# Optimization experiments

Hardware: AMD Instinct MI355X
Metric: run time of the kernel (lower is better)

## Reference

```python
import jax, jax.numpy as jnp
import numpy as np

B, E, CIN, C, PRE, DME, DEN = 8, 64, 128, 128, 128, 32, 32
N_EDGE_TYPES, N_PATH_TYPES = 10, 20


def leaky(v):
    return jnp.where(v >= 0, v, 0.1 * v)


def setup_inputs() -> dict:
    key = jax.random.key(0)
    ks = jax.random.split(key, 30)
    s = 0.05
    inp = {
        'x': jax.random.normal(ks[0], (B, CIN, E), jnp.float32),
        'y': jax.random.normal(ks[1], (B, CIN, E), jnp.float32),
        'm_bias_mat': jax.random.normal(ks[2], (B, E, E), jnp.float32),
        'edge_mat': jax.random.randint(ks[3], (B, E, E), 0, N_EDGE_TYPES),
        'p_bias_mat': jax.random.normal(ks[4], (B, E, E, E), jnp.float32),
        'path_mat': jax.random.randint(ks[5], (B, E, E, E), 0, N_PATH_TYPES),
        'pre_out': jax.random.normal(ks[6], (B, PRE, E, E), jnp.float32),
        # parameters (conv1d/conv2d k=1 weights squeezed to matrices/vectors)
        'xc1_w': jax.random.normal(ks[7], (C, CIN), jnp.float32) * s,
        'yc1_w': jax.random.normal(ks[8], (C, CIN), jnp.float32) * s,
        'xc2_w': jax.random.normal(ks[9], (C,), jnp.float32) * s,
        'xc2_b': jax.random.normal(ks[10], (1,), jnp.float32) * s,
        'yc2_w': jax.random.normal(ks[11], (C,), jnp.float32) * s,
        'yc2_b': jax.random.normal(ks[12], (1,), jnp.float32) * s,
        'pconv_w': jax.random.normal(ks[13], (DEN,), jnp.float32) * s,
        'econv_w': jax.random.normal(ks[14], (DME,), jnp.float32) * s,
        'conv1_w': jax.random.normal(ks[15], (C, 2 * C + PRE), jnp.float32) * s,
        'conv1_b': jax.random.normal(ks[16], (C,), jnp.float32) * s,
        'conv2_w': jax.random.normal(ks[17], (C, C, 3, 3), jnp.float32) * s,
        'conv2_b': jax.random.normal(ks[18], (C,), jnp.float32) * s,
        'score_w': jax.random.normal(ks[19], (C,), jnp.float32) * s,
        'xlin_w': jax.random.normal(ks[20], (CIN, CIN), jnp.float32) * s,
        'ylin_w': jax.random.normal(ks[21], (CIN, CIN), jnp.float32) * s,
        'edge_table': jax.random.normal(ks[22], (N_EDGE_TYPES, DME), jnp.float32) * s,
        'path_table': jax.random.normal(ks[23], (N_PATH_TYPES, DEN), jnp.float32) * s,
    }
    return inp


def reference(x, y, m_bias_mat, edge_mat, p_bias_mat, path_mat, pre_out,
              xc1_w, yc1_w, xc2_w, xc2_b, yc2_w, yc2_b, pconv_w, econv_w,
              conv1_w, conv1_b, conv2_w, conv2_b, score_w, xlin_w, ylin_w,
              edge_table, path_table):
    # x,y: [B, CIN, E]; M == N == entity_num == E (required by path_fea reshape)
    x_f = jnp.einsum('ci,bim->bcm', xc1_w, x)                    # [B,C,M]
    y_f = jnp.einsum('ci,bin->bcn', yc1_w, y)                    # [B,C,N]
    x_self = jnp.einsum('c,bcm->bm', xc2_w, x_f) + xc2_b         # [B,M]
    y_other = jnp.einsum('c,bcn->bn', yc2_w, y_f) + yc2_b        # [B,N]
    # torch broadcast: [B,1,M] + [B,N,1] -> [B,N,M]
    logist = leaky(x_self[:, None, :] + y_other[:, :, None])     # [B,E,E]

    # ---- per-entity path attention (vectorized over entity axis e) ----
    path_embed = path_table[path_mat]                            # [B,E,M,N,DEN]
    path_logist = leaky(jnp.einsum('bemnd,d->bemn', path_embed, pconv_w))
    local = logist[:, None, :, :] + path_logist + p_bias_mat     # [B,E,M,N]
    A = jax.nn.softmax(local, axis=-1)
    x_ret = leaky(jnp.einsum('bemn,bcn->bcem', A, y_f) + x_f[:, :, None, :])  # [B,C,E,M]
    A2 = jax.nn.softmax(jnp.swapaxes(local, 2, 3), axis=-1)
    y_ret = leaky(jnp.einsum('benm,bcm->bcen', A2, x_f) + y_f[:, :, None, :])  # [B,C,E,N]
    path_fea = jnp.concatenate([x_ret, y_ret], axis=1)           # [B,2C,E,E]

    men = jnp.concatenate([path_fea, pre_out], axis=1)           # [B,2C+PRE,E,E]
    h = leaky(jnp.einsum('oc,bcij->boij', conv1_w, men) + conv1_b[None, :, None, None])
    h = jax.lax.conv_general_dilated(h, conv2_w, (1, 1), 'SAME',
                                     dimension_numbers=('NCHW', 'OIHW', 'NCHW'))
    men2rel = leaky(h + conv2_b[None, :, None, None])            # [B,C,E,E]

    scores = leaky(jnp.einsum('c,bcij->bij', score_w, men2rel))  # [B,E,E]
    edge_logist = leaky(jnp.einsum('bmnd,d->bmn', edge_table[edge_mat], econv_w))
    g = logist + scores + edge_logist + m_bias_mat               # [B,E,E]

    x_lin = jnp.einsum('ij,bjm->bmi', xlin_w, x)                 # [B,M,CIN]
    y_lin = jnp.einsum('ij,bjn->bni', ylin_w, y)                 # [B,N,CIN]
    G = jax.nn.softmax(g, axis=-1)
    out_x = jnp.einsum('bmn,bni->bim', G, y_lin) + x             # residual, [B,CIN,M]
    G2 = jax.nn.softmax(jnp.swapaxes(g, 1, 2), axis=-1)
    out_y = jnp.einsum('bnm,bmi->bin', G2, x_lin) + y            # [B,CIN,N]
    return (out_x, out_y, men2rel)
```

## Files before the change

kernel.cpp:

```cpp
#include <hip/hip_runtime.h>
#include <hip/hip_bf16.h>


typedef unsigned short u16;
typedef unsigned int u32;
typedef short s16x8 __attribute__((ext_vector_type(8)));
typedef float f32x4 __attribute__((ext_vector_type(4)));

#define NB 8
#define NE 64
#define NC 128

__device__ __forceinline__ float b2f(u16 u) { return __uint_as_float(((u32)u) << 16); }
__device__ __forceinline__ u16 f2b(float f) {
    u32 x = __float_as_uint(f);
    u32 r = (x + 0x7fffu + ((x >> 16) & 1u)) >> 16;
    return (u16)r;
}
__device__ __forceinline__ float lk(float v) { return v >= 0.f ? v : 0.1f * v; }

__global__ __launch_bounds__(256) void k_prepw(const float* __restrict__ w1, const float* __restrict__ w2,
                                               u16* __restrict__ wA1, u16* __restrict__ wA2) {
    int idx = blockIdx.x * 256 + threadIdx.x;
    if (idx < 49152) {
        int e = idx & 7, lane = (idx >> 3) & 63, mtg = (idx >> 9) & 7, kc = idx >> 12;
        int o = mtg * 16 + (lane & 15), c = kc * 32 + ((lane >> 4) << 3) + e;
        wA1[idx] = f2b(w1[o * 384 + c]);
    } else {
        int id2 = idx - 49152;
        if (id2 < 147456) {
            int e = id2 & 7, lane = (id2 >> 3) & 63, mtg = (id2 >> 9) & 7;
            int kc = (id2 >> 12) & 3, tap = id2 >> 14;
            int o = mtg * 16 + (lane & 15), c = kc * 32 + ((lane >> 4) << 3) + e;
            wA2[id2] = f2b(w2[(o * 128 + c) * 9 + tap]);
        }
    }
}

__global__ __launch_bounds__(64) void k_feat(const float* __restrict__ x, const float* __restrict__ y,
                                             const float* __restrict__ xc1, const float* __restrict__ yc1,
                                             u16* __restrict__ xfb, u16* __restrict__ yfb) {
    int blk = blockIdx.x;
    int which = blk >> 10; int r = blk & 1023;
    int b = r >> 7, c = r & 127;
    const float* in = which ? y : x;
    const float* w = which ? yc1 : xc1;
    u16* out = which ? yfb : xfb;
    int m = threadIdx.x;
    const float* wr = w + c * NC;
    const float* ib = in + b * NC * NE + m;
    float acc = 0.f;
#pragma unroll 8
    for (int i = 0; i < NC; ++i) acc += wr[i] * ib[i * NE];
    out[(b * NC + c) * NE + m] = f2b(acc);
}

__global__ __launch_bounds__(256) void k_transf(const u16* __restrict__ xfb, const u16* __restrict__ yfb,
                                                float* __restrict__ xfT, float* __restrict__ yfT) {
    int blk = blockIdx.x;
    int which = blk >> 3, b = blk & 7;
    const u16* src = which ? yfb : xfb;
    float* dst = which ? yfT : xfT;
    int t = threadIdx.x;
    int m = t >> 2, cq = t & 3;
    for (int o = 0; o < 8; ++o) {
        int c0 = cq * 32 + o * 4;
        float4 v;
        v.x = b2f(src[(b * 128 + c0 + 0) * 64 + m]);
        v.y = b2f(src[(b * 128 + c0 + 1) * 64 + m]);
        v.z = b2f(src[(b * 128 + c0 + 2) * 64 + m]);
        v.w = b2f(src[(b * 128 + c0 + 3) * 64 + m]);
        *(float4*)(dst + (b * 64 + m) * 128 + c0) = v;
    }
}

__global__ __launch_bounds__(128) void k_lin(const float* __restrict__ x, const float* __restrict__ y,
                                             const float* __restrict__ xlw, const float* __restrict__ ylw,
                                             float* __restrict__ xl, float* __restrict__ yl) {
    int blk = blockIdx.x;
    int which = blk >> 9; int r = blk & 511;
    int b = r >> 6, ent = r & 63;
    const float* in = which ? y : x;
    const float* w = which ? ylw : xlw;
    float* out = which ? yl : xl;
    int i = threadIdx.x;
    float acc = 0.f;
#pragma unroll 4
    for (int j = 0; j < NC; ++j) acc += w[i * NC + j] * in[(b * NC + j) * NE + ent];
    out[(b * NE + ent) * NC + i] = acc;
}

__global__ __launch_bounds__(64) void k_selfother(const float* __restrict__ xfT, const float* __restrict__ yfT,
                                                  const float* __restrict__ xc2w, const float* __restrict__ xc2b,
                                                  const float* __restrict__ yc2w, const float* __restrict__ yc2b,
                                                  const float* __restrict__ etab, const float* __restrict__ econv,
                                                  const int* __restrict__ edge_mat, const float* __restrict__ m_bias,
                                                  float* __restrict__ Lw, float* __restrict__ gb) {
    int b = blockIdx.x >> 3, ig = blockIdx.x & 7;
    int t = threadIdx.x;
    __shared__ float sXs[64], sYo[64], sEd[16];
    const float* xr = xfT + (b * 64 + t) * 128;
    const float* yr = yfT + (b * 64 + t) * 128;
    float ax = 0.f, ay = 0.f;
#pragma unroll 4
    for (int c = 0; c < NC; ++c) {
        ax += xc2w[c] * xr[c];
        ay += yc2w[c] * yr[c];
    }
    sXs[t] = ax + xc2b[0];
    sYo[t] = ay + yc2b[0];
    if (t < 10) {
        float s = 0.f;
        for (int d = 0; d < 32; ++d) s += etab[t * 32 + d] * econv[d];
        sEd[t] = lk(s);
    }
    __syncthreads();
    for (int ii = 0; ii < 8; ++ii) {
        int i = ig * 8 + ii;
        int idx = (b * NE + i) * NE + t;
        float L = lk(sXs[t] + sYo[i]);
        Lw[idx] = L;
        gb[idx] = L + sEd[edge_mat[idx]] + m_bias[idx];
    }
}

__global__ __launch_bounds__(256) void k_attn(const float* __restrict__ Lw,
                                              const u16* __restrict__ xfb, const u16* __restrict__ yfb,
                                              const float* __restrict__ xfT, const float* __restrict__ yfT,
                                              const int* __restrict__ path_mat, const float* __restrict__ p_bias,
                                              const float* __restrict__ ptab, const float* __restrict__ pconv,
                                              u16* __restrict__ menT) {
    int b = blockIdx.x >> 6, e = blockIdx.x & 63;
    int t = threadIdx.x;
    int lane = t & 63, w = t >> 6;
    __shared__ float sA[64][68];
    __shared__ u16 Abf[64][72];
    __shared__ u16 E2bf[64][72];
    __shared__ float sRed[256];
    __shared__ float sPdot[20];

    if (t < 20) {
        float s = 0.f;
        for (int d = 0; d < 32; ++d) s += ptab[t * 32 + d] * pconv[d];
        sPdot[t] = lk(s);
    }
    __syncthreads();

    {
        int m = t >> 2, n0 = (t & 3) * 16;
        int base = (((b * 64 + e) * 64 + m) * 64 + n0);
        const int4* pm4 = (const int4*)(path_mat + base);
        const float4* pb4 = (const float4*)(p_bias + base);
        const float4* L4 = (const float4*)(Lw + (b * 64 + m) * 64 + n0);
#pragma unroll
        for (int q = 0; q < 4; ++q) {
            int4 pm = pm4[q]; float4 pb = pb4[q]; float4 l = L4[q];
            float4 v;
            v.x = l.x + sPdot[pm.x] + pb.x;
            v.y = l.y + sPdot[pm.y] + pb.y;
            v.z = l.z + sPdot[pm.z] + pb.z;
            v.w = l.w + sPdot[pm.w] + pb.w;
            *(float4*)&sA[m][n0 + q * 4] = v;
        }
    }
    __syncthreads();

    if (t < 128) {
        int r = t >> 1, h = t & 1;
        const float4* rp = (const float4*)&sA[r][h * 32];
        float mx = -1e30f;
#pragma unroll
        for (int k = 0; k < 8; ++k) {
            float4 v = rp[k];
            mx = fmaxf(mx, fmaxf(fmaxf(v.x, v.y), fmaxf(v.z, v.w)));
        }
        mx = fmaxf(mx, __shfl_xor(mx, 1));
        float s = 0.f;
#pragma unroll
        for (int k = 0; k < 8; ++k) {
            float4 v = rp[k];
            s += __expf(v.x - mx) + __expf(v.y - mx) + __expf(v.z - mx) + __expf(v.w - mx);
        }
        s += __shfl_xor(s, 1);
        if (h == 0) { sRed[r] = mx; sRed[64 + r] = 1.f / s; }
    } else {
        int n = (t - 128) >> 1, h = t & 1;
        float mx = -1e30f;
#pragma unroll
        for (int k = 0; k < 32; ++k) mx = fmaxf(mx, sA[h * 32 + k][n]);
        mx = fmaxf(mx, __shfl_xor(mx, 1));
        float s = 0.f;
#pragma unroll
        for (int k = 0; k < 32; ++k) s += __expf(sA[h * 32 + k][n] - mx);
        s += __shfl_xor(s, 1);
        if (h == 0) { sRed[128 + n] = mx; sRed[192 + n] = 1.f / s; }
    }
    __syncthreads();

    {
        int m = t >> 2, q = t & 3;
        float rmax = sRed[m], rinv = sRed[64 + m];
        const float4* rp = (const float4*)&sA[m][q * 16];
        s16x8 pk[2];
#pragma unroll
        for (int g = 0; g < 2; ++g) {
            float4 v0 = rp[g * 2], v1 = rp[g * 2 + 1];
            pk[g][0] = (short)f2b(__expf(v0.x - rmax) * rinv);
            pk[g][1] = (short)f2b(__expf(v0.y - rmax) * rinv);
            pk[g][2] = (short)f2b(__expf(v0.z - rmax) * rinv);
            pk[g][3] = (short)f2b(__expf(v0.w - rmax) * rinv);
            pk[g][4] = (short)f2b(__expf(v1.x - rmax) * rinv);
            pk[g][5] = (short)f2b(__expf(v1.y - rmax) * rinv);
            pk[g][6] = (short)f2b(__expf(v1.z - rmax) * rinv);
            pk[g][7] = (short)f2b(__expf(v1.w - rmax) * rinv);
            *(s16x8*)&Abf[m][q * 16 + g * 8] = pk[g];
        }
    }
    {
        int n = t >> 2, q = t & 3;
        float cmax = sRed[128 + n], cinv = sRed[192 + n];
        s16x8 pk[2];
#pragma unroll
        for (int g = 0; g < 2; ++g) {
#pragma unroll
            for (int k = 0; k < 8; ++k) {
                float v = sA[q * 16 + g * 8 + k][n];
                pk[g][k] = (short)f2b(__expf(v - cmax) * cinv);
            }
            *(s16x8*)&E2bf[n][q * 16 + g * 8] = pk[g];
        }
    }
    __syncthreads();

    int l15 = lane & 15, q4 = (lane >> 4);
    {
        f32x4 acc[2][4];
#pragma unroll
        for (int ci = 0; ci < 2; ++ci)
#pragma unroll
            for (int mt = 0; mt < 4; ++mt) acc[ci][mt] = (f32x4)(0.f);
#pragma unroll
        for (int kt = 0; kt < 2; ++kt) {
            s16x8 afr[2];
#pragma unroll
            for (int ci = 0; ci < 2; ++ci) {
                int c = (2 * w + ci) * 16 + l15;
                afr[ci] = *(const s16x8*)(yfb + (b * 128 + c) * 64 + kt * 32 + q4 * 8);
            }
            s16x8 bfr[4];
#pragma unroll
            for (int mt = 0; mt < 4; ++mt)
                bfr[mt] = *(const s16x8*)&Abf[mt * 16 + l15][kt * 32 + q4 * 8];
#pragma unroll
            for (int ci = 0; ci < 2; ++ci)
#pragma unroll
                for (int mt = 0; mt < 4; ++mt)
                    acc[ci][mt] = __builtin_amdgcn_mfma_f32_16x16x32_bf16(afr[ci], bfr[mt], acc[ci][mt], 0, 0, 0);
        }
#pragma unroll
        for (int ci = 0; ci < 2; ++ci) {
            int c0 = (2 * w + ci) * 16 + q4 * 4;
#pragma unroll
            for (int mt = 0; mt < 4; ++mt) {
                int m = mt * 16 + l15;
                float4 res = *(const float4*)(xfT + (b * 64 + m) * 128 + c0);
                f32x4 a = acc[ci][mt];
                u32 lo = (u32)f2b(lk(a[0] + res.x)) | ((u32)f2b(lk(a[1] + res.y)) << 16);
                u32 hi = (u32)f2b(lk(a[2] + res.z)) | ((u32)f2b(lk(a[3] + res.w)) << 16);
                *(uint2*)(menT + ((b * 64 + e) * 64 + m) * 384 + c0) = make_uint2(lo, hi);
            }
        }
    }
    {
        f32x4 acc[2][4];
#pragma unroll
        for (int ci = 0; ci < 2; ++ci)
#pragma unroll
            for (int nt = 0; nt < 4; ++nt) acc[ci][nt] = (f32x4)(0.f);
#pragma unroll
        for (int kt = 0; kt < 2; ++kt) {
            s16x8 afr[2];
#pragma unroll
            for (int ci = 0; ci < 2; ++ci) {
                int c = (2 * w + ci) * 16 + l15;
                afr[ci] = *(const s16x8*)(xfb + (b * 128 + c) * 64 + kt * 32 + q4 * 8);
            }
            s16x8 bfr[4];
#pragma unroll
            for (int nt = 0; nt < 4; ++nt)
                bfr[nt] = *(const s16x8*)&E2bf[nt * 16 + l15][kt * 32 + q4 * 8];
#pragma unroll
            for (int ci = 0; ci < 2; ++ci)
#pragma unroll
                for (int nt = 0; nt < 4; ++nt)
                    acc[ci][nt] = __builtin_amdgcn_mfma_f32_16x16x32_bf16(afr[ci], bfr[nt], acc[ci][nt], 0, 0, 0);
        }
#pragma unroll
        for (int ci = 0; ci < 2; ++ci) {
            int c0 = (2 * w + ci) * 16 + q4 * 4;
#pragma unroll
            for (int nt = 0; nt < 4; ++nt) {
                int n = nt * 16 + l15;
                float4 res = *(const float4*)(yfT + (b * 64 + n) * 128 + c0);
                f32x4 a = acc[ci][nt];
                u32 lo = (u32)f2b(lk(a[0] + res.x)) | ((u32)f2b(lk(a[1] + res.y)) << 16);
                u32 hi = (u32)f2b(lk(a[2] + res.z)) | ((u32)f2b(lk(a[3] + res.w)) << 16);
                *(uint2*)(menT + ((b * 64 + e) * 64 + n) * 384 + 128 + c0) = make_uint2(lo, hi);
            }
        }
    }
}

__global__ __launch_bounds__(256) void k_prepre(const float* __restrict__ pre, u16* __restrict__ menT) {
    int b = blockIdx.x >> 6, i = blockIdx.x & 63;
    int t = threadIdx.x;
    int j = t & 63, pg = t >> 6;
#pragma unroll
    for (int oc = 0; oc < 4; ++oc) {
        int p0 = pg * 32 + oc * 8;
        s16x8 v;
#pragma unroll
        for (int k = 0; k < 8; ++k)
            v[k] = (short)f2b(pre[((b * 128 + p0 + k) * 64 + i) * 64 + j]);
        *(s16x8*)(menT + ((b * 64 + i) * 64 + j) * 384 + 256 + p0) = v;
    }
}

__global__ __launch_bounds__(256) void k_conv1(const u16* __restrict__ menT, const u16* __restrict__ wA1,
                                               const float* __restrict__ b1, u16* __restrict__ hT) {
    int b = blockIdx.x >> 6, i = blockIdx.x & 63;
    int t = threadIdx.x;
    int lane = t & 63, w = t >> 6, wm = w & 1, wn = w >> 1;
    int l15 = lane & 15, q4 = lane >> 4;

    f32x4 acc[4][2];
#pragma unroll
    for (int mt = 0; mt < 4; ++mt)
#pragma unroll
        for (int nt = 0; nt < 2; ++nt) acc[mt][nt] = (f32x4)(0.f);

    const u16* mrow = menT + (b * 64 + i) * 64 * 384;
    for (int kc = 0; kc < 12; ++kc) {
        s16x8 af[4];
#pragma unroll
        for (int mt = 0; mt < 4; ++mt)
            af[mt] = *(const s16x8*)(wA1 + (((kc * 8 + wm * 4 + mt) * 64 + lane) << 3));
        s16x8 bf[2];
#pragma unroll
        for (int nt = 0; nt < 2; ++nt) {
            int j = (wn * 2 + nt) * 16 + l15;
            bf[nt] = *(const s16x8*)(mrow + j * 384 + kc * 32 + q4 * 8);
        }
#pragma unroll
        for (int mt = 0; mt < 4; ++mt)
#pragma unroll
            for (int nt = 0; nt < 2; ++nt)
                acc[mt][nt] = __builtin_amdgcn_mfma_f32_16x16x32_bf16(af[mt], bf[nt], acc[mt][nt], 0, 0, 0);
    }

#pragma unroll
    for (int mt = 0; mt < 4; ++mt) {
        int o0 = (wm * 4 + mt) * 16 + q4 * 4;
        float4 bb = *(const float4*)(b1 + o0);
#pragma unroll
        for (int nt = 0; nt < 2; ++nt) {
            int j = (wn * 2 + nt) * 16 + l15;
            f32x4 a = acc[mt][nt];
            u32 lo = (u32)f2b(lk(a[0] + bb.x)) | ((u32)f2b(lk(a[1] + bb.y)) << 16);
            u32 hi = (u32)f2b(lk(a[2] + bb.z)) | ((u32)f2b(lk(a[3] + bb.w)) << 16);
            *(uint2*)(hT + ((b * 64 + i) * 64 + j) * 128 + o0) = make_uint2(lo, hi);
        }
    }
}

__global__ __launch_bounds__(256) void k_conv2(const u16* __restrict__ hT, const u16* __restrict__ wA2,
                                               const float* __restrict__ b2, const float* __restrict__ score_w,
                                               const float* __restrict__ gb, float* __restrict__ m2r,
                                               float* __restrict__ g) {
    int b = blockIdx.x >> 5, ip = blockIdx.x & 31;
    int i0 = ip * 2;
    int t = threadIdx.x;
    int lane = t & 63, w = t >> 6, wm = w & 1, wn = w >> 1;
    __shared__ u16 sB2[4][66][136];
    __shared__ float sSc[2][2][64];

#pragma unroll
    for (int q = 0; q < 2; ++q) {
        int u = q * 256 + t;
        int r = u >> 7, hcol = (u >> 6) & 1, c2 = u & 63;
        *(u32*)&sB2[r][hcol ? 65 : 0][c2 * 2] = 0u;
    }
    for (int it = 0; it < 16; ++it) {
        int u = it * 256 + t;
        int cg = u & 15, j = (u >> 4) & 63, r = u >> 10;
        int ir = i0 - 1 + r;
        int4 v = make_int4(0, 0, 0, 0);
        if (ir >= 0 && ir < 64)
            v = *(const int4*)(hT + ((b * 64 + ir) * 64 + j) * 128 + cg * 8);
        *(int4*)&sB2[r][j + 1][cg * 8] = v;
    }
    __syncthreads();

    f32x4 acc[4][4];
#pragma unroll
    for (int mt = 0; mt < 4; ++mt)
#pragma unroll
        for (int nt = 0; nt < 4; ++nt) acc[mt][nt] = (f32x4)(0.f);

    for (int kc = 0; kc < 4; ++kc) {
#pragma unroll
        for (int tap = 0; tap < 9; ++tap) {
            int di = tap / 3, dj = tap % 3;
            s16x8 af[4];
#pragma unroll
            for (int mt = 0; mt < 4; ++mt)
                af[mt] = *(const s16x8*)(wA2 + ((((tap * 4 + kc) * 8 + wm * 4 + mt) * 64 + lane) << 3));
            int r = wn + di;
#pragma unroll
            for (int nt = 0; nt < 4; ++nt) {
                int jin = nt * 16 + (lane & 15) + dj;
                s16x8 bf = *(const s16x8*)(&sB2[r][jin][kc * 32 + (lane >> 4) * 8]);
#pragma unroll
                for (int mt = 0; mt < 4; ++mt)
                    acc[mt][nt] = __builtin_amdgcn_mfma_f32_16x16x32_bf16(af[mt], bf, acc[mt][nt], 0, 0, 0);
            }
        }
    }

    int i = i0 + wn;
    float part[4] = {0.f, 0.f, 0.f, 0.f};
#pragma unroll
    for (int mt = 0; mt < 4; ++mt) {
        int o0 = wm * 64 + mt * 16 + (lane >> 4) * 4;
        float4 bb = *(const float4*)(b2 + o0);
        float4 sw = *(const float4*)(score_w + o0);
#pragma unroll
        for (int nt = 0; nt < 4; ++nt) {
            int j = nt * 16 + (lane & 15);
            f32x4 a = acc[mt][nt];
            float v0 = lk(a[0] + bb.x), v1 = lk(a[1] + bb.y);
            float v2 = lk(a[2] + bb.z), v3 = lk(a[3] + bb.w);
            float* dst = m2r + ((b * 128 + o0) * 64 + i) * 64 + j;
            dst[0] = v0; dst[4096] = v1; dst[8192] = v2; dst[12288] = v3;
            part[nt] += sw.x * v0 + sw.y * v1 + sw.z * v2 + sw.w * v3;
        }
    }
#pragma unroll
    for (int nt = 0; nt < 4; ++nt) {
        float p = part[nt];
        p += __shfl_xor(p, 16);
        p += __shfl_xor(p, 32);
        if ((lane & 48) == 0) sSc[wm][wn][nt * 16 + lane] = p;
    }
    __syncthreads();
    if (t < 128) {
        int ii = t >> 6, j = t & 63;
        float s = sSc[0][ii][j] + sSc[1][ii][j];
        int gi = (b * 64 + i0 + ii) * 64 + j;
        g[gi] = gb[gi] + lk(s);
    }
}

__global__ __launch_bounds__(128) void k_out(const float* __restrict__ g,
                                             const float* __restrict__ xl, const float* __restrict__ yl,
                                             const float* __restrict__ x, const float* __restrict__ y,
                                             float* __restrict__ out) {
    int blk = blockIdx.x;
    int which = blk >> 9; int r = blk & 511;
    int b = r >> 6, row = r & 63;
    int t = threadIdx.x;
    __shared__ float sW[64];
    if (t < 64) {
        float v = which ? g[(b * 64 + t) * 64 + row] : g[(b * 64 + row) * 64 + t];
        float mx = v;
        for (int off = 32; off > 0; off >>= 1) mx = fmaxf(mx, __shfl_xor(mx, off));
        float e = __expf(v - mx);
        float s = e;
        for (int off = 32; off > 0; off >>= 1) s += __shfl_xor(s, off);
        sW[t] = e / s;
    }
    __syncthreads();
    const float* lin = which ? xl : yl;
    const float* res = which ? y : x;
    float acc = 0.f;
#pragma unroll 4
    for (int k = 0; k < 64; ++k) acc += sW[k] * lin[(b * 64 + k) * NC + t];
    float ov = acc + res[(b * NC + t) * 64 + row];
    out[(which ? 65536 : 0) + (b * NC + t) * 64 + row] = ov;
}

extern "C" void kernel_launch(void* const* d_in, const int* in_sizes, int n_in,
                              void* d_out, int out_size, void* d_ws, size_t ws_size,
                              hipStream_t stream) {
    const float* x = (const float*)d_in[0];
    const float* y = (const float*)d_in[1];
    const float* m_bias = (const float*)d_in[2];
    const int* edge_mat = (const int*)d_in[3];
    const float* p_bias = (const float*)d_in[4];
    const int* path_mat = (const int*)d_in[5];
    const float* pre = (const float*)d_in[6];
    const float* xc1 = (const float*)d_in[7];
    const float* yc1 = (const float*)d_in[8];
    const float* xc2w = (const float*)d_in[9];
    const float* xc2b = (const float*)d_in[10];
    const float* yc2w = (const float*)d_in[11];
    const float* yc2b = (const float*)d_in[12];
    const float* pconv = (const float*)d_in[13];
    const float* econv = (const float*)d_in[14];
    const float* w1 = (const float*)d_in[15];
    const float* b1 = (const float*)d_in[16];
    const float* w2 = (const float*)d_in[17];
    const float* b2 = (const float*)d_in[18];
    const float* score_w = (const float*)d_in[19];
    const float* xlw = (const float*)d_in[20];
    const float* ylw = (const float*)d_in[21];
    const float* etab = (const float*)d_in[22];
    const float* ptab = (const float*)d_in[23];

    float* Lw = (float*)d_ws;
    float* gb = Lw + 32768;
    float* g = gb + 32768;
    float* xfT = g + 32768;
    float* yfT = xfT + 65536;
    float* xl = yfT + 65536;
    float* yl = xl + 65536;
    u16* wA1 = (u16*)(yl + 65536);
    u16* wA2 = wA1 + 49152;
    u16* xfb = wA2 + 147456;
    u16* yfb = xfb + 65536;
    u16* menT = yfb + 65536;
    u16* hT = menT + 12582912;

    float* out = (float*)d_out;
    float* out_m2r = out + 131072;

    hipLaunchKernelGGL(k_prepw, dim3(768), dim3(256), 0, stream, w1, w2, wA1, wA2);
    hipLaunchKernelGGL(k_feat, dim3(2048), dim3(64), 0, stream, x, y, xc1, yc1, xfb, yfb);
    hipLaunchKernelGGL(k_transf, dim3(16), dim3(256), 0, stream, xfb, yfb, xfT, yfT);
    hipLaunchKernelGGL(k_lin, dim3(1024), dim3(128), 0, stream, x, y, xlw, ylw, xl, yl);
    hipLaunchKernelGGL(k_selfother, dim3(64), dim3(64), 0, stream, xfT, yfT, xc2w, xc2b, yc2w, yc2b,
                       etab, econv, edge_mat, m_bias, Lw, gb);
    hipLaunchKernelGGL(k_attn, dim3(512), dim3(256), 0, stream, Lw, xfb, yfb, xfT, yfT,
                       path_mat, p_bias, ptab, pconv, menT);
    hipLaunchKernelGGL(k_prepre, dim3(512), dim3(256), 0, stream, pre, menT);
    hipLaunchKernelGGL(k_conv1, dim3(512), dim3(256), 0, stream, menT, wA1, b1, hT);
    hipLaunchKernelGGL(k_conv2, dim3(256), dim3(256), 0, stream, hT, wA2, b2, score_w, gb,
                       out_m2r, g);
    hipLaunchKernelGGL(k_out, dim3(1024), dim3(128), 0, stream, g, xl, yl, x, y, out);
}
```

Baseline: 213.7 us.

## Fuse front-end projections into MFMA kernel, merge pre copy, retile conv2, MFMA output

Replaces the four scalar front-end kernels (feature conv, transpose, linear, self/other logits) with one per-batch kernel that computes all four projections with bf16 MFMA from LDS-staged transposed inputs. The pre_out copy into menT moves into the attention kernel, which drops a launch. conv2 now handles one row per block with twice as many blocks. The final softmax-weighted sums become a per-batch MFMA kernel. This cuts launches and scalar FMA work, but the front and output kernels run on only 8 blocks, and the linear outputs are now stored in bf16.

```diff
diff --git a/kernel.cpp b/kernel.cpp
--- a/kernel.cpp
+++ b/kernel.cpp
@@ -18,6 +18,13 @@
     return (u16)r;
 }
 __device__ __forceinline__ float lk(float v) { return v >= 0.f ? v : 0.1f * v; }
+__device__ __forceinline__ s16x8 cvt8(const float* p) {
+    float4 a = ((const float4*)p)[0], c = ((const float4*)p)[1];
+    s16x8 r;
+    r[0] = (short)f2b(a.x); r[1] = (short)f2b(a.y); r[2] = (short)f2b(a.z); r[3] = (short)f2b(a.w);
+    r[4] = (short)f2b(c.x); r[5] = (short)f2b(c.y); r[6] = (short)f2b(c.z); r[7] = (short)f2b(c.w);
+    return r;
+}
 
 __global__ __launch_bounds__(256) void k_prepw(const float* __restrict__ w1, const float* __restrict__ w2,
                                                u16* __restrict__ wA1, u16* __restrict__ wA2) {
@@ -37,90 +44,163 @@
     }
 }
 
-__global__ __launch_bounds__(64) void k_feat(const float* __restrict__ x, const float* __restrict__ y,
-                                             const float* __restrict__ xc1, const float* __restrict__ yc1,
-                                             u16* __restrict__ xfb, u16* __restrict__ yfb) {
-    int blk = blockIdx.x;
-    int which = blk >> 10; int r = blk & 1023;
-    int b = r >> 7, c = r & 127;
-    const float* in = which ? y : x;
-    const float* w = which ? yc1 : xc1;
-    u16* out = which ? yfb : xfb;
-    int m = threadIdx.x;
-    const float* wr = w + c * NC;
-    const float* ib = in + b * NC * NE + m;
-    float acc = 0.f;
-#pragma unroll 8
-    for (int i = 0; i < NC; ++i) acc += wr[i] * ib[i * NE];
-    out[(b * NC + c) * NE + m] = f2b(acc);
-}
-
-__global__ __launch_bounds__(256) void k_transf(const u16* __restrict__ xfb, const u16* __restrict__ yfb,
-                                                float* __restrict__ xfT, float* __restrict__ yfT) {
-    int blk = blockIdx.x;
-    int which = blk >> 3, b = blk & 7;
-    const u16* src = which ? yfb : xfb;
-    float* dst = which ? yfT : xfT;
+__global__ __launch_bounds__(256) void k_front(const float* __restrict__ x, const float* __restrict__ y,
+                                               const float* __restrict__ xc1, const float* __restrict__ yc1,
+                                               const float* __restrict__ xc2w, const float* __restrict__ xc2b,
+                                               const float* __restrict__ yc2w, const float* __restrict__ yc2b,
+                                               const float* __restrict__ xlw, const float* __restrict__ ylw,
+                                               const float* __restrict__ etab, const float* __restrict__ econv,
+                                               const int* __restrict__ edge_mat, const float* __restrict__ m_bias,
+                                               u16* __restrict__ xfb, u16* __restrict__ yfb,
+                                               float* __restrict__ xfT, float* __restrict__ yfT,
+                                               u16* __restrict__ xlT, u16* __restrict__ ylT,
+                                               float* __restrict__ Lw, float* __restrict__ gb) {
+    int b = blockIdx.x;
     int t = threadIdx.x;
-    int m = t >> 2, cq = t & 3;
-    for (int o = 0; o < 8; ++o) {
-        int c0 = cq * 32 + o * 4;
-        float4 v;
-        v.x = b2f(src[(b * 128 + c0 + 0) * 64 + m]);
-        v.y = b2f(src[(b * 128 + c0 + 1) * 64 + m]);
-        v.z = b2f(src[(b * 128 + c0 + 2) * 64 + m]);
-        v.w = b2f(src[(b * 128 + c0 + 3) * 64 + m]);
-        *(float4*)(dst + (b * 64 + m) * 128 + c0) = v;
-    }
-}
-
-__global__ __launch_bounds__(128) void k_lin(const float* __restrict__ x, const float* __restrict__ y,
-                                             const float* __restrict__ xlw, const float* __restrict__ ylw,
-                                             float* __restrict__ xl, float* __restrict__ yl) {
-    int blk = blockIdx.x;
-    int which = blk >> 9; int r = blk & 511;
-    int b = r >> 6, ent = r & 63;
-    const float* in = which ? y : x;
-    const float* w = which ? ylw : xlw;
-    float* out = which ? yl : xl;
-    int i = threadIdx.x;
-    float acc = 0.f;
-#pragma unroll 4
-    for (int j = 0; j < NC; ++j) acc += w[i * NC + j] * in[(b * NC + j) * NE + ent];
-    out[(b * NE + ent) * NC + i] = acc;
-}
-
-__global__ __launch_bounds__(64) void k_selfother(const float* __restrict__ xfT, const float* __restrict__ yfT,
-                                                  const float* __restrict__ xc2w, const float* __restrict__ xc2b,
-                                                  const float* __restrict__ yc2w, const float* __restrict__ yc2b,
-                                                  const float* __restrict__ etab, const float* __restrict__ econv,
-                                                  const int* __restrict__ edge_mat, const float* __restrict__ m_bias,
-                                                  float* __restrict__ Lw, float* __restrict__ gb) {
-    int b = blockIdx.x >> 3, ig = blockIdx.x & 7;
-    int t = threadIdx.x;
+    int lane = t & 63, w = t >> 6, l15 = lane & 15, q4 = lane >> 4;
+    __shared__ u16 sxT[64][136];
+    __shared__ u16 syT[64][136];
     __shared__ float sXs[64], sYo[64], sEd[16];
-    const float* xr = xfT + (b * 64 + t) * 128;
-    const float* yr = yfT + (b * 64 + t) * 128;
-    float ax = 0.f, ay = 0.f;
-#pragma unroll 4
-    for (int c = 0; c < NC; ++c) {
-        ax += xc2w[c] * xr[c];
-        ay += yc2w[c] * yr[c];
-    }
-    sXs[t] = ax + xc2b[0];
-    sYo[t] = ay + yc2b[0];
+
     if (t < 10) {
         float s = 0.f;
         for (int d = 0; d < 32; ++d) s += etab[t * 32 + d] * econv[d];
         sEd[t] = lk(s);
     }
-    __syncthreads();
-    for (int ii = 0; ii < 8; ++ii) {
-        int i = ig * 8 + ii;
-        int idx = (b * NE + i) * NE + t;
-        float L = lk(sXs[t] + sYo[i]);
-        Lw[idx] = L;
-        gb[idx] = L + sEd[edge_mat[idx]] + m_bias[idx];
+    {
+        int i = t >> 1, m0 = (t & 1) * 32;
+        const float4* px = (const float4*)(x + (b * 128 + i) * 64 + m0);
+        const float4* py = (const float4*)(y + (b * 128 + i) * 64 + m0);
+#pragma unroll
+        for (int q = 0; q < 8; ++q) {
+            float4 v = px[q];
+            int m = m0 + q * 4;
+            sxT[m + 0][i] = f2b(v.x); sxT[m + 1][i] = f2b(v.y);
+            sxT[m + 2][i] = f2b(v.z); sxT[m + 3][i] = f2b(v.w);
+            float4 u = py[q];
+            syT[m + 0][i] = f2b(u.x); syT[m + 1][i] = f2b(u.y);
+            syT[m + 2][i] = f2b(u.z); syT[m + 3][i] = f2b(u.w);
+        }
+    }
+    __syncthreads();
+
+    int m = w * 16 + l15;
+
+    {
+        f32x4 acc[8];
+#pragma unroll
+        for (int mt = 0; mt < 8; ++mt) acc[mt] = (f32x4)(0.f);
+#pragma unroll
+        for (int kt = 0; kt < 4; ++kt) {
+            s16x8 bfr = *(const s16x8*)&sxT[m][kt * 32 + q4 * 8];
+#pragma unroll
+            for (int mt = 0; mt < 8; ++mt) {
+                s16x8 af = cvt8(xc1 + (mt * 16 + l15) * 128 + kt * 32 + q4 * 8);
+                acc[mt] = __builtin_amdgcn_mfma_f32_16x16x32_bf16(af, bfr, acc[mt], 0, 0, 0);
+            }
+        }
+        float xsp = 0.f;
+#pragma unroll
+        for (int mt = 0; mt < 8; ++mt) {
+            int c0 = mt * 16 + q4 * 4;
+            f32x4 a = acc[mt];
+            xfb[(b * 128 + c0 + 0) * 64 + m] = f2b(a[0]);
+            xfb[(b * 128 + c0 + 1) * 64 + m] = f2b(a[1]);
+            xfb[(b * 128 + c0 + 2) * 64 + m] = f2b(a[2]);
+            xfb[(b * 128 + c0 + 3) * 64 + m] = f2b(a[3]);
+            *(float4*)(xfT + (b * 64 + m) * 128 + c0) = make_float4(a[0], a[1], a[2], a[3]);
+            float4 wv = *(const float4*)(xc2w + c0);
+            xsp += wv.x * a[0] + wv.y * a[1] + wv.z * a[2] + wv.w * a[3];
+        }
+        xsp += __shfl_xor(xsp, 16);
+        xsp += __shfl_xor(xsp, 32);
+        if (q4 == 0) sXs[m] = xsp + xc2b[0];
+    }
+    {
+        f32x4 acc[8];
+#pragma unroll
+        for (int mt = 0; mt < 8; ++mt) acc[mt] = (f32x4)(0.f);
+#pragma unroll
+        for (int kt = 0; kt < 4; ++kt) {
+            s16x8 bfr = *(const s16x8*)&syT[m][kt * 32 + q4 * 8];
+#pragma unroll
+            for (int mt = 0; mt < 8; ++mt) {
+                s16x8 af = cvt8(yc1 + (mt * 16 + l15) * 128 + kt * 32 + q4 * 8);
+                acc[mt] = __builtin_amdgcn_mfma_f32_16x16x32_bf16(af, bfr, acc[mt], 0, 0, 0);
+            }
+        }
+        float ysp = 0.f;
+#pragma unroll
+        for (int mt = 0; mt < 8; ++mt) {
+            int c0 = mt * 16 + q4 * 4;
+            f32x4 a = acc[mt];
+            yfb[(b * 128 + c0 + 0) * 64 + m] = f2b(a[0]);
+            yfb[(b * 128 + c0 + 1) * 64 + m] = f2b(a[1]);
+            yfb[(b * 128 + c0 + 2) * 64 + m] = f2b(a[2]);
+            yfb[(b * 128 + c0 + 3) * 64 + m] = f2b(a[3]);
+            *(float4*)(yfT + (b * 64 + m) * 128 + c0) = make_float4(a[0], a[1], a[2], a[3]);
+            float4 wv = *(const float4*)(yc2w + c0);
+            ysp += wv.x * a[0] + wv.y * a[1] + wv.z * a[2] + wv.w * a[3];
+        }
+        ysp += __shfl_xor(ysp, 16);
+        ysp += __shfl_xor(ysp, 32);
+        if (q4 == 0) sYo[m] = ysp + yc2b[0];
+    }
+    {
+        f32x4 acc[8];
+#pragma unroll
+        for (int mt = 0; mt < 8; ++mt) acc[mt] = (f32x4)(0.f);
+#pragma unroll
+        for (int kt = 0; kt < 4; ++kt) {
+            s16x8 bfr = *(const s16x8*)&sxT[m][kt * 32 + q4 * 8];
+#pragma unroll
+            for (int mt = 0; mt < 8; ++mt) {
+                s16x8 af = cvt8(xlw + (mt * 16 + l15) * 128 + kt * 32 + q4 * 8);
+                acc[mt] = __builtin_amdgcn_mfma_f32_16x16x32_bf16(af, bfr, acc[mt], 0, 0, 0);
+            }
+        }
+#pragma unroll
+        for (int mt = 0; mt < 8; ++mt) {
+            int i0 = mt * 16 + q4 * 4;
+            f32x4 a = acc[mt];
+            xlT[(b * 128 + i0 + 0) * 64 + m] = f2b(a[0]);
+            xlT[(b * 128 + i0 + 1) * 64 + m] = f2b(a[1]);
+            xlT[(b * 128 + i0 + 2) * 64 + m] = f2b(a[2]);
+            xlT[(b * 128 + i0 + 3) * 64 + m] = f2b(a[3]);
+        }
+    }
+    {
+        f32x4 acc[8];
+#pragma unroll
+        for (int mt = 0; mt < 8; ++mt) acc[mt] = (f32x4)(0.f);
+#pragma unroll
+        for (int kt = 0; kt < 4; ++kt) {
+            s16x8 bfr = *(const s16x8*)&syT[m][kt * 32 + q4 * 8];
+#pragma unroll
+            for (int mt = 0; mt < 8; ++mt) {
+                s16x8 af = cvt8(ylw + (mt * 16 + l15) * 128 + kt * 32 + q4 * 8);
+                acc[mt] = __builtin_amdgcn_mfma_f32_16x16x32_bf16(af, bfr, acc[mt], 0, 0, 0);
+            }
+        }
+#pragma unroll
+        for (int mt = 0; mt < 8; ++mt) {
+            int i0 = mt * 16 + q4 * 4;
+            f32x4 a = acc[mt];
+            ylT[(b * 128 + i0 + 0) * 64 + m] = f2b(a[0]);
+            ylT[(b * 128 + i0 + 1) * 64 + m] = f2b(a[1]);
+            ylT[(b * 128 + i0 + 2) * 64 + m] = f2b(a[2]);
+            ylT[(b * 128 + i0 + 3) * 64 + m] = f2b(a[3]);
+        }
+    }
+    __syncthreads();
+#pragma unroll
+    for (int r = 0; r < 16; ++r) {
+        int idx = r * 256 + t;
+        int i = idx >> 6, j = idx & 63;
+        int gidx = b * 4096 + idx;
+        float L = lk(sXs[j] + sYo[i]);
+        Lw[gidx] = L;
+        gb[gidx] = L + sEd[edge_mat[gidx]] + m_bias[gidx];
     }
 }
 
@@ -129,7 +209,7 @@
                                               const float* __restrict__ xfT, const float* __restrict__ yfT,
                                               const int* __restrict__ path_mat, const float* __restrict__ p_bias,
                                               const float* __restrict__ ptab, const float* __restrict__ pconv,
-                                              u16* __restrict__ menT) {
+                                              const float* __restrict__ pre, u16* __restrict__ menT) {
     int b = blockIdx.x >> 6, e = blockIdx.x & 63;
     int t = threadIdx.x;
     int lane = t & 63, w = t >> 6;
@@ -201,38 +281,38 @@
         int m = t >> 2, q = t & 3;
         float rmax = sRed[m], rinv = sRed[64 + m];
         const float4* rp = (const float4*)&sA[m][q * 16];
-        s16x8 pk[2];
-#pragma unroll
-        for (int g = 0; g < 2; ++g) {
-            float4 v0 = rp[g * 2], v1 = rp[g * 2 + 1];
-            pk[g][0] = (short)f2b(__expf(v0.x - rmax) * rinv);
-            pk[g][1] = (short)f2b(__expf(v0.y - rmax) * rinv);
-            pk[g][2] = (short)f2b(__expf(v0.z - rmax) * rinv);
-            pk[g][3] = (short)f2b(__expf(v0.w - rmax) * rinv);
-            pk[g][4] = (short)f2b(__expf(v1.x - rmax) * rinv);
-            pk[g][5] = (short)f2b(__expf(v1.y - rmax) * rinv);
-            pk[g][6] = (short)f2b(__expf(v1.z - rmax) * rinv);
-            pk[g][7] = (short)f2b(__expf(v1.w - rmax) * rinv);
-            *(s16x8*)&Abf[m][q * 16 + g * 8] = pk[g];
+#pragma unroll
+        for (int g2 = 0; g2 < 2; ++g2) {
+            float4 v0 = rp[g2 * 2], v1 = rp[g2 * 2 + 1];
+            s16x8 pk;
+            pk[0] = (short)f2b(__expf(v0.x - rmax) * rinv);
+            pk[1] = (short)f2b(__expf(v0.y - rmax) * rinv);
+            pk[2] = (short)f2b(__expf(v0.z - rmax) * rinv);
+            pk[3] = (short)f2b(__expf(v0.w - rmax) * rinv);
+            pk[4] = (short)f2b(__expf(v1.x - rmax) * rinv);
+            pk[5] = (short)f2b(__expf(v1.y - rmax) * rinv);
+            pk[6] = (short)f2b(__expf(v1.z - rmax) * rinv);
+            pk[7] = (short)f2b(__expf(v1.w - rmax) * rinv);
+            *(s16x8*)&Abf[m][q * 16 + g2 * 8] = pk;
         }
     }
     {
         int n = t >> 2, q = t & 3;
         float cmax = sRed[128 + n], cinv = sRed[192 + n];
-        s16x8 pk[2];
-#pragma unroll
-        for (int g = 0; g < 2; ++g) {
+#pragma unroll
+        for (int g2 = 0; g2 < 2; ++g2) {
+            s16x8 pk;
 #pragma unroll
             for (int k = 0; k < 8; ++k) {
-                float v = sA[q * 16 + g * 8 + k][n];
-                pk[g][k] = (short)f2b(__expf(v - cmax) * cinv);
-            }
-            *(s16x8*)&E2bf[n][q * 16 + g * 8] = pk[g];
-        }
-    }
-    __syncthreads();
-
-    int l15 = lane & 15, q4 = (lane >> 4);
+                float v = sA[q * 16 + g2 * 8 + k][n];
+                pk[k] = (short)f2b(__expf(v - cmax) * cinv);
+            }
+            *(s16x8*)&E2bf[n][q * 16 + g2 * 8] = pk;
+        }
+    }
+    __syncthreads();
+
+    int l15 = lane & 15, q4 = lane >> 4;
     {
         f32x4 acc[2][4];
 #pragma unroll
@@ -309,20 +389,17 @@
             }
         }
     }
-}
-
-__global__ __launch_bounds__(256) void k_prepre(const float* __restrict__ pre, u16* __restrict__ menT) {
-    int b = blockIdx.x >> 6, i = blockIdx.x & 63;
-    int t = threadIdx.x;
-    int j = t & 63, pg = t >> 6;
-#pragma unroll
-    for (int oc = 0; oc < 4; ++oc) {
-        int p0 = pg * 32 + oc * 8;
-        s16x8 v;
-#pragma unroll
-        for (int k = 0; k < 8; ++k)
-            v[k] = (short)f2b(pre[((b * 128 + p0 + k) * 64 + i) * 64 + j]);
-        *(s16x8*)(menT + ((b * 64 + i) * 64 + j) * 384 + 256 + p0) = v;
+    {
+        int j = t & 63, pg = t >> 6;
+#pragma unroll
+        for (int oc = 0; oc < 4; ++oc) {
+            int p0 = pg * 32 + oc * 8;
+            s16x8 v;
+#pragma unroll
+            for (int k = 0; k < 8; ++k)
+                v[k] = (short)f2b(pre[((b * 128 + p0 + k) * 64 + e) * 64 + j]);
+            *(s16x8*)(menT + ((b * 64 + e) * 64 + j) * 384 + 256 + p0) = v;
+        }
     }
 }
 
@@ -377,23 +454,26 @@
                                                const float* __restrict__ b2, const float* __restrict__ score_w,
                                                const float* __restrict__ gb, float* __restrict__ m2r,
                                                float* __restrict__ g) {
-    int b = blockIdx.x >> 5, ip = blockIdx.x & 31;
-    int i0 = ip * 2;
+    int b = blockIdx.x >> 6, i = blockIdx.x & 63;
     int t = threadIdx.x;
     int lane = t & 63, w = t >> 6, wm = w & 1, wn = w >> 1;
-    __shared__ u16 sB2[4][66][136];
-    __shared__ float sSc[2][2][64];
+    int l15 = lane & 15, q4 = lane >> 4;
+    __shared__ u16 sB2[3][66][136];
+    __shared__ float sSc[2][64];
 
 #pragma unroll
     for (int q = 0; q < 2; ++q) {
         int u = q * 256 + t;
-        int r = u >> 7, hcol = (u >> 6) & 1, c2 = u & 63;
-        *(u32*)&sB2[r][hcol ? 65 : 0][c2 * 2] = 0u;
-    }
-    for (int it = 0; it < 16; ++it) {
+        if (u < 384) {
+            int r = u >> 7, rem = u & 127, hcol = rem >> 6, c2 = rem & 63;
+            *(u32*)&sB2[r][hcol ? 65 : 0][c2 * 2] = 0u;
+        }
+    }
+#pragma unroll
+    for (int it = 0; it < 12; ++it) {
         int u = it * 256 + t;
         int cg = u & 15, j = (u >> 4) & 63, r = u >> 10;
-        int ir = i0 - 1 + r;
+        int ir = i - 1 + r;
         int4 v = make_int4(0, 0, 0, 0);
         if (ir >= 0 && ir < 64)
             v = *(const int4*)(hT + ((b * 64 + ir) * 64 + j) * 128 + cg * 8);
@@ -401,11 +481,11 @@
     }
     __syncthreads();
 
-    f32x4 acc[4][4];
+    f32x4 acc[4][2];
 #pragma unroll
     for (int mt = 0; mt < 4; ++mt)
 #pragma unroll
-        for (int nt = 0; nt < 4; ++nt) acc[mt][nt] = (f32x4)(0.f);
+        for (int nt = 0; nt < 2; ++nt) acc[mt][nt] = (f32x4)(0.f);
 
     for (int kc = 0; kc < 4; ++kc) {
 #pragma unroll
@@ -415,11 +495,10 @@
 #pragma unroll
             for (int mt = 0; mt < 4; ++mt)
                 af[mt] = *(const s16x8*)(wA2 + ((((tap * 4 + kc) * 8 + wm * 4 + mt) * 64 + lane) << 3));
-            int r = wn + di;
-#pragma unroll
-            for (int nt = 0; nt < 4; ++nt) {
-                int jin = nt * 16 + (lane & 15) + dj;
-                s16x8 bf = *(const s16x8*)(&sB2[r][jin][kc * 32 + (lane >> 4) * 8]);
+#pragma unroll
+            for (int nt = 0; nt < 2; ++nt) {
+                int jin = wn * 32 + nt * 16 + l15 + dj;
+                s16x8 bf = *(const s16x8*)(&sB2[di][jin][kc * 32 + q4 * 8]);
 #pragma unroll
                 for (int mt = 0; mt < 4; ++mt)
                     acc[mt][nt] = __builtin_amdgcn_mfma_f32_16x16x32_bf16(af[mt], bf, acc[mt][nt], 0, 0, 0);
@@ -427,16 +506,15 @@
         }
     }
 
-    int i = i0 + wn;
-    float part[4] = {0.f, 0.f, 0.f, 0.f};
+    float part[2] = {0.f, 0.f};
 #pragma unroll
     for (int mt = 0; mt < 4; ++mt) {
-        int o0 = wm * 64 + mt * 16 + (lane >> 4) * 4;
+        int o0 = wm * 64 + mt * 16 + q4 * 4;
         float4 bb = *(const float4*)(b2 + o0);
         float4 sw = *(const float4*)(score_w + o0);
 #pragma unroll
-        for (int nt = 0; nt < 4; ++nt) {
-            int j = nt * 16 + (lane & 15);
+        for (int nt = 0; nt < 2; ++nt) {
+            int j = wn * 32 + nt * 16 + l15;
             f32x4 a = acc[mt][nt];
             float v0 = lk(a[0] + bb.x), v1 = lk(a[1] + bb.y);
             float v2 = lk(a[2] + bb.z), v3 = lk(a[3] + bb.w);
@@ -446,47 +524,155 @@
         }
     }
 #pragma unroll
-    for (int nt = 0; nt < 4; ++nt) {
+    for (int nt = 0; nt < 2; ++nt) {
         float p = part[nt];
         p += __shfl_xor(p, 16);
         p += __shfl_xor(p, 32);
-        if ((lane & 48) == 0) sSc[wm][wn][nt * 16 + lane] = p;
-    }
-    __syncthreads();
+        if (q4 == 0) sSc[wm][wn * 32 + nt * 16 + l15] = p;
+    }
+    __syncthreads();
+    if (t < 64) {
+        float s = sSc[0][t] + sSc[1][t];
+        int gi = (b * 64 + i) * 64 + t;
+        g[gi] = gb[gi] + lk(s);
+    }
+}
+
+__global__ __launch_bounds__(256) void k_gout(const float* __restrict__ g,
+                                              const u16* __restrict__ xlT, const u16* __restrict__ ylT,
+                                              const float* __restrict__ x, const float* __restrict__ y,
+                                              float* __restrict__ out) {
+    int b = blockIdx.x;
+    int t = threadIdx.x;
+    int lane = t & 63, w = t >> 6, l15 = lane & 15, q4 = lane >> 4;
+    __shared__ float sG[64][68];
+    __shared__ u16 Gbf[64][72];
+    __shared__ u16 G2bf[64][72];
+    __shared__ float sRed[256];
+
+#pragma unroll
+    for (int r = 0; r < 16; ++r) {
+        int idx = r * 256 + t;
+        sG[idx >> 6][idx & 63] = g[b * 4096 + idx];
+    }
+    __syncthreads();
+
     if (t < 128) {
-        int ii = t >> 6, j = t & 63;
-        float s = sSc[0][ii][j] + sSc[1][ii][j];
-        int gi = (b * 64 + i0 + ii) * 64 + j;
-        g[gi] = gb[gi] + lk(s);
-    }
-}
-
-__global__ __launch_bounds__(128) void k_out(const float* __restrict__ g,
-                                             const float* __restrict__ xl, const float* __restrict__ yl,
-                                             const float* __restrict__ x, const float* __restrict__ y,
-                                             float* __restrict__ out) {
-    int blk = blockIdx.x;
-    int which = blk >> 9; int r = blk & 511;
-    int b = r >> 6, row = r & 63;
-    int t = threadIdx.x;
-    __shared__ float sW[64];
-    if (t < 64) {
-        float v = which ? g[(b * 64 + t) * 64 + row] : g[(b * 64 + row) * 64 + t];
-        float mx = v;
-        for (int off = 32; off > 0; off >>= 1) mx = fmaxf(mx, __shfl_xor(mx, off));
-        float e = __expf(v - mx);
-        float s = e;
-        for (int off = 32; off > 0; off >>= 1) s += __shfl_xor(s, off);
-        sW[t] = e / s;
-    }
-    __syncthreads();
-    const float* lin = which ? xl : yl;
-    const float* res = which ? y : x;
-    float acc = 0.f;
-#pragma unroll 4
-    for (int k = 0; k < 64; ++k) acc += sW[k] * lin[(b * 64 + k) * NC + t];
-    float ov = acc + res[(b * NC + t) * 64 + row];
-    out[(which ? 65536 : 0) + (b * NC + t) * 64 + row] = ov;
+        int r = t >> 1, h = t & 1;
+        const float4* rp = (const float4*)&sG[r][h * 32];
+        float mx = -1e30f;
+#pragma unroll
+        for (int k = 0; k < 8; ++k) {
+            float4 v = rp[k];
+            mx = fmaxf(mx, fmaxf(fmaxf(v.x, v.y), fmaxf(v.z, v.w)));
+        }
+        mx = fmaxf(mx, __shfl_xor(mx, 1));
+        float s = 0.f;
+#pragma unroll
+        for (int k = 0; k < 8; ++k) {
+            float4 v = rp[k];
+            s += __expf(v.x - mx) + __expf(v.y - mx) + __expf(v.z - mx) + __expf(v.w - mx);
+        }
+        s += __shfl_xor(s, 1);
+        if (h == 0) { sRed[r] = mx; sRed[64 + r] = 1.f / s; }
+    } else {
+        int n = (t - 128) >> 1, h = t & 1;
+        float mx = -1e30f;
+#pragma unroll
+        for (int k = 0; k < 32; ++k) mx = fmaxf(mx, sG[h * 32 + k][n]);
+        mx = fmaxf(mx, __shfl_xor(mx, 1));
+        float s = 0.f;
+#pragma unroll
+        for (int k = 0; k < 32; ++k) s += __expf(sG[h * 32 + k][n] - mx);
+        s += __shfl_xor(s, 1);
+        if (h == 0) { sRed[128 + n] = mx; sRed[192 + n] = 1.f / s; }
+    }
+    __syncthreads();
+
+    {
+        int m = t >> 2, q = t & 3;
+        float rmax = sRed[m], rinv = sRed[64 + m];
+        const float4* rp = (const float4*)&sG[m][q * 16];
+#pragma unroll
+        for (int g2 = 0; g2 < 2; ++g2) {
+            float4 v0 = rp[g2 * 2], v1 = rp[g2 * 2 + 1];
+            s16x8 pk;
+            pk[0] = (short)f2b(__expf(v0.x - rmax) * rinv);
+            pk[1] = (short)f2b(__expf(v0.y - rmax) * rinv);
+            pk[2] = (short)f2b(__expf(v0.z - rmax) * rinv);
+            pk[3] = (short)f2b(__expf(v0.w - rmax) * rinv);
+            pk[4] = (short)f2b(__expf(v1.x - rmax) * rinv);
+            pk[5] = (short)f2b(__expf(v1.y - rmax) * rinv);
+            pk[6] = (short)f2b(__expf(v1.z - rmax) * rinv);
+            pk[7] = (short)f2b(__expf(v1.w - rmax) * rinv);
+            *(s16x8*)&Gbf[m][q * 16 + g2 * 8] = pk;
+        }
+    }
+    {
+        int n = t >> 2, q = t & 3;
+        float cmax = sRed[128 + n], cinv = sRed[192 + n];
+#pragma unroll
+        for (int g2 = 0; g2 < 2; ++g2) {
+            s16x8 pk;
+#pragma unroll
+            for (int k = 0; k < 8; ++k) {
+                float v = sG[q * 16 + g2 * 8 + k][n];
+                pk[k] = (short)f2b(__expf(v - cmax) * cinv);
+            }
+            *(s16x8*)&G2bf[n][q * 16 + g2 * 8] = pk;
+        }
+    }
+    __syncthreads();
+
+    int mcol = w * 16 + l15;
+    {
+        f32x4 acc[8];
+#pragma unroll
+        for (int mt = 0; mt < 8; ++mt) acc[mt] = (f32x4)(0.f);
+#pragma unroll
+        for (int kt = 0; kt < 2; ++kt) {
+            s16x8 bfr = *(const s16x8*)&Gbf[mcol][kt * 32 + q4 * 8];
+#pragma unroll
+            for (int mt = 0; mt < 8; ++mt) {
+                s16x8 af = *(const s16x8*)(ylT + (b * 128 + mt * 16 + l15) * 64 + kt * 32 + q4 * 8);
+                acc[mt] = __builtin_amdgcn_mfma_f32_16x16x32_bf16(af, bfr, acc[mt], 0, 0, 0);
+            }
+        }
+#pragma unroll
+        for (int mt = 0; mt < 8; ++mt) {
+            int i0 = mt * 16 + q4 * 4;
+            f32x4 a = acc[mt];
+#pragma unroll
+            for (int r = 0; r < 4; ++r) {
+                int ad = (b * 128 + i0 + r) * 64 + mcol;
+                out[ad] = a[r] + x[ad];
+            }
+        }
+    }
+    {
+        f32x4 acc[8];
+#pragma unroll
+        for (int mt = 0; mt < 8; ++mt) acc[mt] = (f32x4)(0.f);
+#pragma unroll
+        for (int kt = 0; kt < 2; ++kt) {
+            s16x8 bfr = *(const s16x8*)&G2bf[mcol][kt * 32 + q4 * 8];
+#pragma unroll
+            for (int mt = 0; mt < 8; ++mt) {
+                s16x8 af = *(const s16x8*)(xlT + (b * 128 + mt * 16 + l15) * 64 + kt * 32 + q4 * 8);
+                acc[mt] = __builtin_amdgcn_mfma_f32_16x16x32_bf16(af, bfr, acc[mt], 0, 0, 0);
+            }
+        }
+#pragma unroll
+        for (int mt = 0; mt < 8; ++mt) {
+            int i0 = mt * 16 + q4 * 4;
+            f32x4 a = acc[mt];
+#pragma unroll
+            for (int r = 0; r < 4; ++r) {
+                int ad = (b * 128 + i0 + r) * 64 + mcol;
+                out[65536 + ad] = a[r] + y[ad];
+            }
+        }
+    }
 }
 
 extern "C" void kernel_launch(void* const* d_in, const int* in_sizes, int n_in,
@@ -522,29 +708,26 @@
     float* g = gb + 32768;
     float* xfT = g + 32768;
     float* yfT = xfT + 65536;
-    float* xl = yfT + 65536;
-    float* yl = xl + 65536;
-    u16* wA1 = (u16*)(yl + 65536);
+    u16* wA1 = (u16*)(yfT + 65536);
     u16* wA2 = wA1 + 49152;
     u16* xfb = wA2 + 147456;
     u16* yfb = xfb + 65536;
-    u16* menT = yfb + 65536;
+    u16* xlT = yfb + 65536;
+    u16* ylT = xlT + 65536;
+    u16* menT = ylT + 65536;
     u16* hT = menT + 12582912;
 
     float* out = (float*)d_out;
     float* out_m2r = out + 131072;
 
     hipLaunchKernelGGL(k_prepw, dim3(768), dim3(256), 0, stream, w1, w2, wA1, wA2);
-    hipLaunchKernelGGL(k_feat, dim3(2048), dim3(64), 0, stream, x, y, xc1, yc1, xfb, yfb);
-    hipLaunchKernelGGL(k_transf, dim3(16), dim3(256), 0, stream, xfb, yfb, xfT, yfT);
-    hipLaunchKernelGGL(k_lin, dim3(1024), dim3(128), 0, stream, x, y, xlw, ylw, xl, yl);
-    hipLaunchKernelGGL(k_selfother, dim3(64), dim3(64), 0, stream, xfT, yfT, xc2w, xc2b, yc2w, yc2b,
-                       etab, econv, edge_mat, m_bias, Lw, gb);
+    hipLaunchKernelGGL(k_front, dim3(8), dim3(256), 0, stream, x, y, xc1, yc1, xc2w, xc2b,
+                       yc2w, yc2b, xlw, ylw, etab, econv, edge_mat, m_bias,
+                       xfb, yfb, xfT, yfT, xlT, ylT, Lw, gb);
     hipLaunchKernelGGL(k_attn, dim3(512), dim3(256), 0, stream, Lw, xfb, yfb, xfT, yfT,
-                       path_mat, p_bias, ptab, pconv, menT);
-    hipLaunchKernelGGL(k_prepre, dim3(512), dim3(256), 0, stream, pre, menT);
+                       path_mat, p_bias, ptab, pconv, pre, menT);
     hipLaunchKernelGGL(k_conv1, dim3(512), dim3(256), 0, stream, menT, wA1, b1, hT);
-    hipLaunchKernelGGL(k_conv2, dim3(256), dim3(256), 0, stream, hT, wA2, b2, score_w, gb,
+    hipLaunchKernelGGL(k_conv2, dim3(512), dim3(256), 0, stream, hT, wA2, b2, score_w, gb,
                        out_m2r, g);
-    hipLaunchKernelGGL(k_out, dim3(1024), dim3(128), 0, stream, g, xl, yl, x, y, out);
-}
+    hipLaunchKernelGGL(k_gout, dim3(8), dim3(256), 0, stream, g, xlT, ylT, x, y, out);
+}
```

New measurement: 219.0 us. 1.02x slower.
